# Optimization experiments

Measured on AMD Instinct MI355X. Metric: run time of the kernel, lower is better.

The kernel has to match this reference:

```python
import jax, jax.numpy as jnp
import numpy as np

B, T, ENC, DEC = 512, 500, 1024, 1024

def setup_inputs() -> dict:
    key = jax.random.key(0)
    k1, k2, k3, k4 = jax.random.split(key, 4)
    decoderFeature = jax.random.normal(k1, (B, DEC), dtype=jnp.float32)
    encoderFeature = jax.random.normal(k2, (B, T, ENC), dtype=jnp.float32)
    skill_net_lengths = jax.random.randint(k3, (B,), 1, T + 1, dtype=jnp.int32)
    W = jax.random.normal(k4, (ENC, DEC), dtype=jnp.float32) * (6.0 / (ENC + DEC)) ** 0.5
    return {"decoderFeature": decoderFeature, "encoderFeature": encoderFeature,
            "skill_net_lengths": skill_net_lengths, "W": W}

def reference(decoderFeature, encoderFeature, skill_net_lengths, W):
    # subResult = F.linear(decoderFeature, W) -> [B, ENC]
    sub = decoderFeature @ W.T
    # attn scores: bmm([B,1,ENC], [B,ENC,T]) -> [B, T]
    scores = jnp.einsum('be,bte->bt', sub, encoderFeature)
    valid = jnp.arange(T)[None, :] < skill_net_lengths[:, None]  # [B, T]
    scores = jnp.where(valid, scores, -jnp.inf)
    attn = jax.nn.softmax(scores, axis=-1)  # [B, T]
    sumResult = jnp.einsum('bt,bte->be', attn, encoderFeature)  # [B, ENC]
    return attn[:, None, :], sumResult
```

## Files before the change

kernel.cpp:

```cpp
#include <hip/hip_runtime.h>
#include <math.h>

#define B 512
#define T 500
#define ENC 1024
#define DEC 1024

#define GM 32
#define GN 64
#define GK 16

__global__ __launch_bounds__(256) void gemm_sub(
    const float* __restrict__ A,
    const float* __restrict__ Wm,
    float* __restrict__ C)
{
    __shared__ float As[GK][GM + 2];
    __shared__ float Bs[GK][GN + 4];

    const int tid = threadIdx.x;
    const int bm0 = blockIdx.y * GM;
    const int bn0 = blockIdx.x * GN;

    const int tx = tid & 15;
    const int ty = tid >> 4;

    float accr[2][4] = {{0.f,0.f,0.f,0.f},{0.f,0.f,0.f,0.f}};

    const int arow = tid >> 3;
    const int acol = (tid & 7) * 2;
    const int brow = tid >> 2;
    const int bcol = (tid & 3) * 4;

    const float* aptr = A  + (size_t)(bm0 + arow) * DEC + acol;
    const float* bptr = Wm + (size_t)(bn0 + brow) * DEC + bcol;

    float2 a2 = *(const float2*)(aptr);
    float4 b4 = *(const float4*)(bptr);

    for (int k0 = 0; k0 < DEC; k0 += GK) {
        As[acol][arow]     = a2.x;
        As[acol + 1][arow] = a2.y;
        Bs[bcol][brow]     = b4.x;
        Bs[bcol + 1][brow] = b4.y;
        Bs[bcol + 2][brow] = b4.z;
        Bs[bcol + 3][brow] = b4.w;
        __syncthreads();

        if (k0 + GK < DEC) {
            a2 = *(const float2*)(aptr + k0 + GK);
            b4 = *(const float4*)(bptr + k0 + GK);
        }

#pragma unroll
        for (int k = 0; k < GK; k++) {
            float2 av = *(const float2*)&As[k][ty * 2];
            float4 bv = *(const float4*)&Bs[k][tx * 4];
            accr[0][0] = fmaf(av.x, bv.x, accr[0][0]);
            accr[0][1] = fmaf(av.x, bv.y, accr[0][1]);
            accr[0][2] = fmaf(av.x, bv.z, accr[0][2]);
            accr[0][3] = fmaf(av.x, bv.w, accr[0][3]);
            accr[1][0] = fmaf(av.y, bv.x, accr[1][0]);
            accr[1][1] = fmaf(av.y, bv.y, accr[1][1]);
            accr[1][2] = fmaf(av.y, bv.z, accr[1][2]);
            accr[1][3] = fmaf(av.y, bv.w, accr[1][3]);
        }
        __syncthreads();
    }

    float4 c0 = make_float4(accr[0][0], accr[0][1], accr[0][2], accr[0][3]);
    float4 c1 = make_float4(accr[1][0], accr[1][1], accr[1][2], accr[1][3]);
    *(float4*)(C + (size_t)(bm0 + ty * 2) * ENC + bn0 + tx * 4)     = c0;
    *(float4*)(C + (size_t)(bm0 + ty * 2 + 1) * ENC + bn0 + tx * 4) = c1;
}

#define NW 8
#define BLK (NW * 64)

#define LOADROW(E, TT) do {                                            \
    const float* _p = encb + (size_t)(TT) * ENC + 4 * lane;            \
    float4 _v0 = *(const float4*)(_p);                                 \
    float4 _v1 = *(const float4*)(_p + 256);                           \
    float4 _v2 = *(const float4*)(_p + 512);                           \
    float4 _v3 = *(const float4*)(_p + 768);                           \
    E[0]=_v0.x;  E[1]=_v0.y;  E[2]=_v0.z;  E[3]=_v0.w;                 \
    E[4]=_v1.x;  E[5]=_v1.y;  E[6]=_v1.z;  E[7]=_v1.w;                 \
    E[8]=_v2.x;  E[9]=_v2.y;  E[10]=_v2.z; E[11]=_v2.w;                \
    E[12]=_v3.x; E[13]=_v3.y; E[14]=_v3.z; E[15]=_v3.w;                \
} while (0)

#define LOADPAIR(E0, E1, TT) do {                                      \
    LOADROW(E0, TT);                                                   \
    if ((TT) + 1 < len) LOADROW(E1, (TT) + 1);                         \
} while (0)

#define PROCESS_PAIR(E0, E1, TT) do {                                  \
    const bool _r1 = ((TT) + 1 < len);                                 \
    if (!_r1) {                                                        \
        _Pragma("unroll")                                              \
        for (int _i = 0; _i < 16; _i++) E1[_i] = 0.f;                  \
    }                                                                  \
    float _d0a = 0.f, _d0b = 0.f, _d1a = 0.f, _d1b = 0.f;              \
    _Pragma("unroll")                                                  \
    for (int _i = 0; _i < 16; _i += 2) {                               \
        _d0a = fmaf(E0[_i],     sub_r[_i],     _d0a);                  \
        _d0b = fmaf(E0[_i + 1], sub_r[_i + 1], _d0b);                  \
        _d1a = fmaf(E1[_i],     sub_r[_i],     _d1a);                  \
        _d1b = fmaf(E1[_i + 1], sub_r[_i + 1], _d1b);                  \
    }                                                                  \
    float _d0 = _d0a + _d0b;                                           \
    float _d1 = _d1a + _d1b;                                           \
    _Pragma("unroll")                                                  \
    for (int _off = 32; _off > 0; _off >>= 1) {                        \
        _d0 += __shfl_xor(_d0, _off, 64);                              \
        _d1 += __shfl_xor(_d1, _off, 64);                              \
    }                                                                  \
    if (lane == 0) {                                                   \
        lds_scores[(TT)] = _d0;                                        \
        if (_r1) lds_scores[(TT) + 1] = _d1;                           \
    }                                                                  \
    const float _d1e = _r1 ? _d1 : -INFINITY;                          \
    const float _md  = fmaxf(_d0, _d1e);                               \
    if (_md > m) {                                                     \
        const float _al = __expf(m - _md);          \
        const float _p0 = __expf(_d0 - _md);                           \
        const float _p1 = _r1 ? __expf(_d1 - _md) : 0.f;               \
        l = fmaf(l, _al, _p0 + _p1);                                   \
        _Pragma("unroll")                                              \
        for (int _i = 0; _i < 16; _i++)                                \
            acc[_i] = fmaf(acc[_i], _al,                               \
                           fmaf(_p0, E0[_i], _p1 * E1[_i]));           \
        m = _md;                                                       \
    } else {                                                           \
        const float _p0 = __expf(_d0 - m);                             \
        const float _p1 = _r1 ? __expf(_d1 - m) : 0.f;                 \
        l += _p0 + _p1;                                                \
        _Pragma("unroll")                                              \
        for (int _i = 0; _i < 16; _i++)                                \
            acc[_i] = fmaf(_p1, E1[_i], fmaf(_p0, E0[_i], acc[_i]));   \
    }                                                                  \
} while (0)

__global__ __launch_bounds__(BLK, 4) void attn_fused(
    const float* __restrict__ sub,
    const float* __restrict__ enc,
    const int* __restrict__ lens,
    float* __restrict__ out_attn,
    float* __restrict__ out_sum)
{
    __shared__ float lds_scores[T];
    __shared__ float lds_m[NW];
    __shared__ float lds_l[NW];
    __shared__ float lds_o[NW][ENC];

    const int b    = blockIdx.x;
    const int tid  = threadIdx.x;
    const int wave = tid >> 6;
    const int lane = tid & 63;
    const int len  = lens[b];

    const float* encb = enc + (size_t)b * T * ENC;
    const float* subb = sub + (size_t)b * ENC;

    float sub_r[16];
#pragma unroll
    for (int c = 0; c < 4; c++) {
        float4 s4 = *(const float4*)(subb + c * 256 + 4 * lane);
        sub_r[c * 4 + 0] = s4.x; sub_r[c * 4 + 1] = s4.y;
        sub_r[c * 4 + 2] = s4.z; sub_r[c * 4 + 3] = s4.w;
    }

    float acc[16];
#pragma unroll
    for (int i = 0; i < 16; i++) acc[i] = 0.f;
    float m = -INFINITY;
    float l = 0.f;

    int t = 2 * wave;
    if (t < len) {
        float eA0[16], eA1[16], eB0[16], eB1[16];
        LOADPAIR(eA0, eA1, t);
        for (;;) {
            const int tB = t + 2 * NW;
            const bool vB = (tB < len);
            if (vB) LOADPAIR(eB0, eB1, tB);
            PROCESS_PAIR(eA0, eA1, t);
            if (!vB) break;
            const int tA = tB + 2 * NW;
            const bool vA = (tA < len);
            if (vA) LOADPAIR(eA0, eA1, tA);
            PROCESS_PAIR(eB0, eB1, tB);
            if (!vA) break;
            t = tA;
        }
    }

    if (lane == 0) { lds_m[wave] = m; lds_l[wave] = l; }
#pragma unroll
    for (int c = 0; c < 4; c++) {
        float4 v = make_float4(acc[c * 4 + 0], acc[c * 4 + 1],
                               acc[c * 4 + 2], acc[c * 4 + 3]);
        *(float4*)&lds_o[wave][c * 256 + 4 * lane] = v;
    }
    __syncthreads();

    float mg = -INFINITY;
#pragma unroll
    for (int w = 0; w < NW; w++) mg = fmaxf(mg, lds_m[w]);
    float scale[NW];
    float lg = 0.f;
#pragma unroll
    for (int w = 0; w < NW; w++) {
        float mw = lds_m[w];
        float s  = (mw == -INFINITY) ? 0.f : __expf(mw - mg);
        scale[w] = s;
        lg = fmaf(lds_l[w], s, lg);
    }
    const float inv_l = 1.f / lg;

    const int e0 = 2 * tid;
    float o0 = 0.f, o1 = 0.f;
#pragma unroll
    for (int w = 0; w < NW; w++) {
        o0 = fmaf(scale[w], lds_o[w][e0], o0);
        o1 = fmaf(scale[w], lds_o[w][e0 + 1], o1);
    }
    *(float2*)(out_sum + (size_t)b * ENC + e0) = make_float2(o0 * inv_l, o1 * inv_l);

    for (int tt = tid; tt < T; tt += BLK) {
        float v = 0.f;
        if (tt < len) v = __expf(lds_scores[tt] - mg) * inv_l;
        out_attn[(size_t)b * T + tt] = v;
    }
}

extern "C" void kernel_launch(void* const* d_in, const int* in_sizes, int n_in,
                              void* d_out, int out_size, void* d_ws, size_t ws_size,
                              hipStream_t stream) {
    const float* dec  = (const float*)d_in[0];
    const float* enc  = (const float*)d_in[1];
    const int*   lens = (const int*)d_in[2];
    const float* Wm   = (const float*)d_in[3];

    float* out       = (float*)d_out;
    float* out_attn  = out;
    float* out_sum   = out + (size_t)B * T;
    float* sub       = (float*)d_ws;

    gemm_sub<<<dim3(16, 16), 256, 0, stream>>>(dec, Wm, sub);
    attn_fused<<<dim3(B), BLK, 0, stream>>>(sub, enc, lens, out_attn, out_sum);
}
```

Before: 1.260 ms.

## Split attention over time into two halves with a separate combine kernel

The fused attention kernel now runs two blocks per batch row, each covering half of the time steps. Each block writes its partial max, sum, weighted output and raw scores to workspace. A new combine kernel merges the two halves and produces the normalized attention and summed output. This doubles the block count to balance the variable sequence lengths and fill more CUs, at the cost of an extra launch and a round trip of partial results through workspace.

New measurement: 1.267 ms. Within noise of the previous version (+0.6%).

```diff
diff --git a/kernel.cpp b/kernel.cpp
--- a/kernel.cpp
+++ b/kernel.cpp
@@ -76,6 +76,7 @@
 
 #define NW 8
 #define BLK (NW * 64)
+#define HALF_T 250
 
 #define LOADROW(E, TT) do {                                            \
     const float* _p = encb + (size_t)(TT) * ENC + 4 * lane;            \
@@ -91,11 +92,11 @@
 
 #define LOADPAIR(E0, E1, TT) do {                                      \
     LOADROW(E0, TT);                                                   \
-    if ((TT) + 1 < len) LOADROW(E1, (TT) + 1);                         \
+    if ((TT) + 1 < tend) LOADROW(E1, (TT) + 1);                        \
 } while (0)
 
 #define PROCESS_PAIR(E0, E1, TT) do {                                  \
-    const bool _r1 = ((TT) + 1 < len);                                 \
+    const bool _r1 = ((TT) + 1 < tend);                                \
     if (!_r1) {                                                        \
         _Pragma("unroll")                                              \
         for (int _i = 0; _i < 16; _i++) E1[_i] = 0.f;                  \
@@ -116,8 +117,8 @@
         _d1 += __shfl_xor(_d1, _off, 64);                              \
     }                                                                  \
     if (lane == 0) {                                                   \
-        lds_scores[(TT)] = _d0;                                        \
-        if (_r1) lds_scores[(TT) + 1] = _d1;                           \
+        lds_scores[(TT) - tbase] = _d0;                                \
+        if (_r1) lds_scores[(TT) + 1 - tbase] = _d1;                   \
     }                                                                  \
     const float _d1e = _r1 ? _d1 : -INFINITY;                          \
     const float _md  = fmaxf(_d0, _d1e);                               \
@@ -141,24 +142,30 @@
     }                                                                  \
 } while (0)
 
-__global__ __launch_bounds__(BLK, 4) void attn_fused(
+__global__ __launch_bounds__(BLK, 4) void attn_part(
     const float* __restrict__ sub,
     const float* __restrict__ enc,
     const int* __restrict__ lens,
-    float* __restrict__ out_attn,
-    float* __restrict__ out_sum)
+    float* __restrict__ scores_ws,
+    float* __restrict__ part_m,
+    float* __restrict__ part_l,
+    float* __restrict__ part_o)
 {
-    __shared__ float lds_scores[T];
+    __shared__ float lds_scores[HALF_T];
     __shared__ float lds_m[NW];
     __shared__ float lds_l[NW];
     __shared__ float lds_o[NW][ENC];
 
-    const int b    = blockIdx.x;
+    const int b    = blockIdx.x >> 1;
+    const int half = blockIdx.x & 1;
     const int tid  = threadIdx.x;
     const int wave = tid >> 6;
     const int lane = tid & 63;
     const int len  = lens[b];
 
+    const int tbase = half * HALF_T;
+    const int tend  = (len < tbase + HALF_T) ? len : (tbase + HALF_T);
+
     const float* encb = enc + (size_t)b * T * ENC;
     const float* subb = sub + (size_t)b * ENC;
 
@@ -176,18 +183,18 @@
     float m = -INFINITY;
     float l = 0.f;
 
-    int t = 2 * wave;
-    if (t < len) {
+    int t = tbase + 2 * wave;
+    if (t < tend) {
         float eA0[16], eA1[16], eB0[16], eB1[16];
         LOADPAIR(eA0, eA1, t);
         for (;;) {
             const int tB = t + 2 * NW;
-            const bool vB = (tB < len);
+            const bool vB = (tB < tend);
             if (vB) LOADPAIR(eB0, eB1, tB);
             PROCESS_PAIR(eA0, eA1, t);
             if (!vB) break;
             const int tA = tB + 2 * NW;
-            const bool vA = (tA < len);
+            const bool vA = (tA < tend);
             if (vA) LOADPAIR(eA0, eA1, tA);
             PROCESS_PAIR(eB0, eB1, tB);
             if (!vA) break;
@@ -216,7 +223,6 @@
         scale[w] = s;
         lg = fmaf(lds_l[w], s, lg);
     }
-    const float inv_l = 1.f / lg;
 
     const int e0 = 2 * tid;
     float o0 = 0.f, o1 = 0.f;
@@ -225,11 +231,55 @@
         o0 = fmaf(scale[w], lds_o[w][e0], o0);
         o1 = fmaf(scale[w], lds_o[w][e0 + 1], o1);
     }
-    *(float2*)(out_sum + (size_t)b * ENC + e0) = make_float2(o0 * inv_l, o1 * inv_l);
-
-    for (int tt = tid; tt < T; tt += BLK) {
+    *(float2*)(part_o + (size_t)(half * B + b) * ENC + e0) = make_float2(o0, o1);
+
+    if (tid == 0) {
+        part_m[half * B + b] = mg;
+        part_l[half * B + b] = lg;
+    }
+
+    const int vcount = tend - tbase;
+    for (int i = tid; i < vcount; i += BLK)
+        scores_ws[(size_t)b * T + tbase + i] = lds_scores[i];
+}
+
+__global__ __launch_bounds__(256) void attn_combine(
+    const float* __restrict__ scores_ws,
+    const float* __restrict__ part_m,
+    const float* __restrict__ part_l,
+    const float* __restrict__ part_o,
+    const int* __restrict__ lens,
+    float* __restrict__ out_attn,
+    float* __restrict__ out_sum)
+{
+    const int b   = blockIdx.x;
+    const int tid = threadIdx.x;
+    const int len = lens[b];
+
+    const float m0 = part_m[b];
+    const float m1 = part_m[B + b];
+    const float l0 = part_l[b];
+    const float l1 = part_l[B + b];
+
+    const float mg = fmaxf(m0, m1);
+    const float s0 = (m0 == -INFINITY) ? 0.f : __expf(m0 - mg);
+    const float s1 = (m1 == -INFINITY) ? 0.f : __expf(m1 - mg);
+    const float lg = fmaf(l0, s0, l1 * s1);
+    const float inv_l = 1.f / lg;
+
+    const int e0 = 4 * tid;
+    float4 a = *(const float4*)(part_o + (size_t)b * ENC + e0);
+    float4 c = *(const float4*)(part_o + (size_t)(B + b) * ENC + e0);
+    float4 r;
+    r.x = fmaf(s0, a.x, s1 * c.x) * inv_l;
+    r.y = fmaf(s0, a.y, s1 * c.y) * inv_l;
+    r.z = fmaf(s0, a.z, s1 * c.z) * inv_l;
+    r.w = fmaf(s0, a.w, s1 * c.w) * inv_l;
+    *(float4*)(out_sum + (size_t)b * ENC + e0) = r;
+
+    for (int tt = tid; tt < T; tt += 256) {
         float v = 0.f;
-        if (tt < len) v = __expf(lds_scores[tt] - mg) * inv_l;
+        if (tt < len) v = __expf(scores_ws[(size_t)b * T + tt] - mg) * inv_l;
         out_attn[(size_t)b * T + tt] = v;
     }
 }
@@ -245,8 +295,17 @@
     float* out       = (float*)d_out;
     float* out_attn  = out;
     float* out_sum   = out + (size_t)B * T;
-    float* sub       = (float*)d_ws;
+
+    float* ws        = (float*)d_ws;
+    float* sub       = ws;
+    float* scores_ws = sub + (size_t)B * ENC;
+    float* part_m    = scores_ws + (size_t)B * T;
+    float* part_l    = part_m + 2 * B;
+    float* part_o    = part_l + 2 * B;
 
     gemm_sub<<<dim3(16, 16), 256, 0, stream>>>(dec, Wm, sub);
-    attn_fused<<<dim3(B), BLK, 0, stream>>>(sub, enc, lens, out_attn, out_sum);
+    attn_part<<<dim3(2 * B), BLK, 0, stream>>>(sub, enc, lens, scores_ws,
+                                               part_m, part_l, part_o);
+    attn_combine<<<dim3(B), 256, 0, stream>>>(scores_ws, part_m, part_l,
+                                              part_o, lens, out_attn, out_sum);
 }
```
